# Kernel optimization log

Hardware: AMD Instinct MI355X
Metric: run time of the kernel (lower is better)

## Reference

```python
import jax, jax.numpy as jnp
import numpy as np

ONE_HOT_MAX_SIZES = [1, 4, 8, 16] * 16  # 64 features, total param width = 480
MIN_SIGMA = 1e-4
MIN_PROB = 1e-4
BATCH = 65536
WIDTH = sum(2 if s <= 1 else s for s in ONE_HOT_MAX_SIZES)  # 480


def setup_inputs() -> dict:
    key = jax.random.key(0)
    distr_params = jax.random.normal(key, (BATCH, WIDTH), dtype=jnp.float32)
    return {"distr_params": distr_params}


def reference(distr_params):
    # sample_most_probable=True: Gaussian -> mean, Categorical -> argmax class.
    # Static Python loop over the fixed, structurally-distinct feature columns;
    # XLA fuses the resulting thin slices into one pass.
    cols = []
    c = 0
    for size in ONE_HOT_MAX_SIZES:
        if size <= 1:
            params = distr_params[:, c:c + 2]  # [B, 2] = (mu, sigma_params)
            c += 2
            mu = params[:, :1]                 # mean of Normal(mu, softplus(sig))
            cols.append(mu)
        else:
            params = distr_params[:, c:c + size]          # [B, size]
            c += size
            probs = jax.nn.softmax(params, axis=-1)
            probs = jnp.clip(probs, MIN_PROB)
            probs = probs / probs.sum(-1, keepdims=True)  # renormalize
            idx = jnp.argmax(probs, axis=1)[:, None].astype(jnp.float32)
            cols.append(idx)
    return jnp.concatenate(cols, axis=1)  # [B, n_features] = [65536, 64]
```

## Files before the change

### kernel.cpp

```cpp
#include <hip/hip_runtime.h>


constexpr int WIDTH   = 480;
constexpr int NOUT    = 64;
constexpr int WAVES   = 4;
constexpr int RPW     = 4;
constexpr int RPB     = WAVES * RPW;
constexpr int THREADS = WAVES * 64;

__device__ __forceinline__ void async_cp16(const float* g, float* l) {
    __builtin_amdgcn_global_load_lds(
        (const __attribute__((address_space(1))) void*)g,
        (__attribute__((address_space(3))) void*)l, 16, 0, 0);
}
__device__ __forceinline__ void async_cp4(const float* g, float* l) {
    __builtin_amdgcn_global_load_lds(
        (const __attribute__((address_space(1))) void*)g,
        (__attribute__((address_space(3))) void*)l, 4, 0, 0);
}

template <int N>
__device__ __forceinline__ float argmaxN(const float* __restrict__ p) {
    float best = p[0];
    int   bi   = 0;
#pragma unroll
    for (int i = 1; i < N; ++i) {
        if (p[i] > best) { best = p[i]; bi = i; }
    }
    return (float)bi;
}

__global__ __launch_bounds__(THREADS)
void gcs_kernel(const float* __restrict__ in, float* __restrict__ out) {
    __shared__ float lds[WAVES * RPW * WIDTH];

    const int wid  = threadIdx.x >> 6;
    const int lane = threadIdx.x & 63;

    const size_t tile_row0 = (size_t)blockIdx.x * RPB + wid * RPW;
    const float* gsrc  = in + tile_row0 * WIDTH;
    float*       lbase = &lds[wid * RPW * WIDTH];

#pragma unroll
    for (int k = 0; k < 7; ++k)
        async_cp16(gsrc + k * 256 + lane * 4, lbase + k * 256 + lane * 4);
    async_cp4(gsrc + 1792 + lane, lbase + 1792 + lane);
    async_cp4(gsrc + 1856 + lane, lbase + 1856 + lane);

    asm volatile("s_waitcnt vmcnt(0)" ::: "memory");

    const int r = lane >> 4;
    const int h = lane & 15;
    const float2* w2 = reinterpret_cast<const float2*>(lbase + r * WIDTH + h * 30);

    float v[30];
#pragma unroll
    for (int i = 0; i < 15; ++i) {
        float2 t = w2[i];
        v[2 * i]     = t.x;
        v[2 * i + 1] = t.y;
    }

    float4 o;
    o.x = v[0];
    o.y = argmaxN<4>(v + 2);
    o.z = argmaxN<8>(v + 6);
    o.w = argmaxN<16>(v + 14);

    *reinterpret_cast<float4*>(out + (tile_row0 + r) * NOUT + h * 4) = o;
}

extern "C" void kernel_launch(void* const* d_in, const int* in_sizes, int n_in,
                              void* d_out, int out_size, void* d_ws, size_t ws_size,
                              hipStream_t stream) {
    const float* in  = (const float*)d_in[0];
    float*       out = (float*)d_out;

    int batch  = in_sizes[0] / WIDTH;
    int blocks = batch / RPB;

    gcs_kernel<<<blocks, THREADS, 0, stream>>>(in, out);
}
```

Baseline: 26.53 us.

## Double-buffer per-wave LDS tiles so each wave processes four tiles

Each wave now handles four consecutive 4-row tiles instead of one. It uses two LDS buffers so the async global-to-LDS copy of the next tile is in flight while the current tile is reduced, with partial vmcnt waits. The grid shrinks by a factor of four and LDS per block doubles, which lowers the number of resident blocks per CU. That may reduce memory-level parallelism in a kernel that is already bandwidth bound.

```diff
diff --git a/kernel.cpp b/kernel.cpp
--- a/kernel.cpp
+++ b/kernel.cpp
@@ -3,10 +3,11 @@
 
 constexpr int WIDTH   = 480;
 constexpr int NOUT    = 64;
+constexpr int RPW     = 4;
+constexpr int TPW     = 4;
 constexpr int WAVES   = 4;
-constexpr int RPW     = 4;
-constexpr int RPB     = WAVES * RPW;
 constexpr int THREADS = WAVES * 64;
+constexpr int TILE_F  = RPW * WIDTH;
 
 __device__ __forceinline__ void async_cp16(const float* g, float* l) {
     __builtin_amdgcn_global_load_lds(
@@ -17,6 +18,14 @@
     __builtin_amdgcn_global_load_lds(
         (const __attribute__((address_space(1))) void*)g,
         (__attribute__((address_space(3))) void*)l, 4, 0, 0);
+}
+
+__device__ __forceinline__ void stage_tile(const float* g, float* l, int lane) {
+#pragma unroll
+    for (int k = 0; k < 7; ++k)
+        async_cp16(g + k * 256 + lane * 4, l + k * 256 + lane * 4);
+    async_cp4(g + 1792 + lane, l + 1792 + lane);
+    async_cp4(g + 1856 + lane, l + 1856 + lane);
 }
 
 template <int N>
@@ -30,25 +39,8 @@
     return (float)bi;
 }
 
-__global__ __launch_bounds__(THREADS)
-void gcs_kernel(const float* __restrict__ in, float* __restrict__ out) {
-    __shared__ float lds[WAVES * RPW * WIDTH];
-
-    const int wid  = threadIdx.x >> 6;
-    const int lane = threadIdx.x & 63;
-
-    const size_t tile_row0 = (size_t)blockIdx.x * RPB + wid * RPW;
-    const float* gsrc  = in + tile_row0 * WIDTH;
-    float*       lbase = &lds[wid * RPW * WIDTH];
-
-#pragma unroll
-    for (int k = 0; k < 7; ++k)
-        async_cp16(gsrc + k * 256 + lane * 4, lbase + k * 256 + lane * 4);
-    async_cp4(gsrc + 1792 + lane, lbase + 1792 + lane);
-    async_cp4(gsrc + 1856 + lane, lbase + 1856 + lane);
-
-    asm volatile("s_waitcnt vmcnt(0)" ::: "memory");
-
+__device__ __forceinline__ void compute_store(const float* lbase, float* out,
+                                              size_t row_base, int lane) {
     const int r = lane >> 4;
     const int h = lane & 15;
     const float2* w2 = reinterpret_cast<const float2*>(lbase + r * WIDTH + h * 30);
@@ -67,7 +59,37 @@
     o.z = argmaxN<8>(v + 6);
     o.w = argmaxN<16>(v + 14);
 
-    *reinterpret_cast<float4*>(out + (tile_row0 + r) * NOUT + h * 4) = o;
+    *reinterpret_cast<float4*>(out + (row_base + r) * NOUT + h * 4) = o;
+}
+
+__global__ __launch_bounds__(THREADS)
+void gcs_kernel(const float* __restrict__ in, float* __restrict__ out) {
+    __shared__ float lds[WAVES * 2 * TILE_F];
+
+    const int wid  = threadIdx.x >> 6;
+    const int lane = threadIdx.x & 63;
+
+    const size_t gw   = (size_t)blockIdx.x * WAVES + wid;
+    const size_t row0 = gw * (RPW * TPW);
+    const float* gsrc = in + row0 * WIDTH;
+
+    float* buf0 = &lds[wid * 2 * TILE_F];
+    float* buf1 = buf0 + TILE_F;
+
+    stage_tile(gsrc, buf0, lane);
+
+#pragma unroll
+    for (int t = 0; t < TPW; ++t) {
+        float* cur = (t & 1) ? buf1 : buf0;
+        float* nxt = (t & 1) ? buf0 : buf1;
+        if (t + 1 < TPW) {
+            stage_tile(gsrc + (t + 1) * TILE_F, nxt, lane);
+            asm volatile("s_waitcnt vmcnt(9)" ::: "memory");
+        } else {
+            asm volatile("s_waitcnt vmcnt(1)" ::: "memory");
+        }
+        compute_store(cur, out, row0 + (size_t)t * RPW, lane);
+    }
 }
 
 extern "C" void kernel_launch(void* const* d_in, const int* in_sizes, int n_in,
@@ -77,7 +99,7 @@
     float*       out = (float*)d_out;
 
     int batch  = in_sizes[0] / WIDTH;
-    int blocks = batch / RPB;
+    int blocks = batch / (RPW * TPW * WAVES);
 
     gcs_kernel<<<blocks, THREADS, 0, stream>>>(in, out);
 }
```

Result: faster. 25.81 us (-2.7%).
